# Optimization experiments

Measured on AMD Instinct MI355X. Metric: run time of the kernel, lower is better.

## Reference

```python
import jax, jax.numpy as jnp
import numpy as np

E, C_IN, NUM_CLASSES = 4, 3, 100
HW = 32
C1, C2, GC = 64, 128, 16
FC_IN = C2 * (HW // 4) * (HW // 4)  # 128*8*8 = 8192


def _conv(x, w, b):
    # x: [B,Cin,H,W], w: [Cout,Cin,3,3] -> [B,Cout,H,W] (SAME padding)
    y = jax.lax.conv_general_dilated(x, w, (1, 1), 'SAME',
                                     dimension_numbers=('NCHW', 'OIHW', 'NCHW'))
    return y + b[None, :, None, None]


def _maxpool2(x):
    return jax.lax.reduce_window(x, -jnp.inf, jax.lax.max,
                                 (1, 1, 2, 2), (1, 1, 2, 2), 'VALID')


def setup_inputs() -> dict:
    key = jax.random.key(0)
    ks = jax.random.split(key, 12)
    s = lambda k, shape, fan: (jax.random.normal(k, shape, jnp.float32) / np.sqrt(fan))
    return {
        'x': jax.random.normal(ks[0], (1024, C_IN, HW, HW), jnp.float32),
        # gating network
        'gate_cw': s(ks[1], (GC, C_IN, 3, 3), C_IN * 9),
        'gate_cb': jnp.zeros((GC,), jnp.float32),
        'gate_fw': s(ks[2], (E, GC), GC),
        'gate_fb': jnp.zeros((E,), jnp.float32),
        # stacked expert params [E, ...]
        'e_c1w': s(ks[3], (E, C1, C_IN, 3, 3), C_IN * 9),
        'e_c1b': jnp.zeros((E, C1), jnp.float32),
        'e_c2w': s(ks[4], (E, C2, C1, 3, 3), C1 * 9),
        'e_c2b': jnp.zeros((E, C2), jnp.float32),
        'e_fw': s(ks[5], (E, NUM_CLASSES, FC_IN), FC_IN),
        'e_fb': jnp.zeros((E, NUM_CLASSES), jnp.float32),
    }


def reference(x, gate_cw, gate_cb, gate_fw, gate_fb,
              e_c1w, e_c1b, e_c2w, e_c2b, e_fw, e_fb):
    B = x.shape[0]
    # --- gating: conv -> relu -> global avg pool -> linear -> softmax ---
    g = jax.nn.relu(_conv(x, gate_cw, gate_cb))            # [B,GC,H,W]
    g = g.mean(axis=(2, 3))                                # [B,GC]
    router_probs = jax.nn.softmax(g @ gate_fw.T + gate_fb) # [B,E]

    best_weights = router_probs.max(axis=1)                # [B]
    best_indices = jnp.argmax(router_probs, axis=1)        # [B]

    # --- hard top-1 dispatch: mask-and-combine (same math as gather/scatter) ---
    final_output = jnp.zeros((B, NUM_CLASSES), x.dtype)
    for e in range(E):  # fixed small expert count, structurally distinct params
        h = jax.nn.relu(_conv(x, e_c1w[e], e_c1b[e]))      # [B,64,32,32]
        h = _maxpool2(h)                                   # [B,64,16,16]
        h = jax.nn.relu(_conv(h, e_c2w[e], e_c2b[e]))      # [B,128,16,16]
        h = _maxpool2(h)                                   # [B,128,8,8]
        logits = h.reshape(B, -1) @ e_fw[e].T + e_fb[e]    # [B,100]
        mask = (best_indices == e)[:, None]
        final_output = final_output + jnp.where(
            mask, logits * best_weights[:, None], 0.0)

    mean_probs = router_probs.mean(axis=0)
    aux_loss = jnp.mean((mean_probs - 1.0 / E) ** 2)
    return final_output, router_probs, aux_loss
```

## Files before the change

kernel.cpp:

```cpp
#include <hip/hip_runtime.h>
#include <hip/hip_bf16.h>
#include <cstdint>


#define B_TOT 1024

typedef __attribute__((ext_vector_type(8))) short short8;
typedef __attribute__((ext_vector_type(16))) float f32x16;

__device__ __forceinline__ ushort f2bf(float f) {
  uint32_t u = __float_as_uint(f);
  u += 0x7fffu + ((u >> 16) & 1u);
  return (ushort)(u >> 16);
}

__global__ __launch_bounds__(256) void k_wprep(const float* __restrict__ w2,
                                               ushort* __restrict__ wp) {
  const int i = blockIdx.x * 256 + threadIdx.x;
  const int j = i & 7;
  const int cout = (i >> 3) & 127;
  const int kb = (i >> 10) & 7;
  const int kkE = i >> 13;
  const int kk = kkE - (kkE / 9) * 9;
  const int e = kkE / 9;
  const int ci = kb * 8 + j;
  const float f = w2[(size_t)(((e * 128 + cout) * 64 + ci) * 9) + kk];
  wp[i] = f2bf(f);
}

__global__ __launch_bounds__(256) void k_w1prep(const float* __restrict__ w1,
                                                ushort* __restrict__ wA) {
  const int i = blockIdx.x * 256 + threadIdx.x;
  const int j = i & 7;
  const int cout = (i >> 3) & 63;
  const int kb = (i >> 9) & 3;
  const int e = i >> 11;
  const int k = kb * 8 + j;
  float f = 0.f;
  if (k < 27) {
    const int ci = k / 9;
    const int kk = k - ci * 9;
    f = w1[(size_t)(((e * 64 + cout) * 3 + ci) * 9) + kk];
  }
  wA[i] = f2bf(f);
}

__global__ __launch_bounds__(256) void k_wfc(const float* __restrict__ efw,
                                             ushort* __restrict__ wfc) {
  const int i = blockIdx.x * 256 + threadIdx.x;
  const int j = i & 7;
  const int cout = (i >> 3) & 127;
  const int kb = (i >> 10) & 1023;
  const int e = i >> 20;
  const int k = kb * 8 + j;
  float f = 0.f;
  if (cout < 100) f = efw[((size_t)(e * 100 + cout)) * 8192 + k];
  wfc[i] = f2bf(f);
}

__global__ __launch_bounds__(256, 2) void k_gate(
    const float* __restrict__ x, const float* __restrict__ gcw,
    const float* __restrict__ gcb, float* __restrict__ g_mean) {
  __shared__ float xs[3 * 34 * 34];
  __shared__ float red[4 * 16];
  const int b = blockIdx.x;
  const int t = threadIdx.x;
  const float* xb = x + (size_t)b * 3072;

  for (int c = t; c < 3468; c += 256) {
    const int ci = c / 1156;
    const int rem = c - ci * 1156;
    const int y = rem / 34;
    const int xx = rem - y * 34;
    const int gy = y - 1, gx = xx - 1;
    float v = 0.f;
    if (gy >= 0 && gy < 32 && gx >= 0 && gx < 32) v = xb[ci * 1024 + gy * 32 + gx];
    xs[c] = v;
  }
  __syncthreads();

  const int r = t >> 3;
  const int c0 = (t & 7) * 4;

  float accp[16][4];
#pragma unroll
  for (int c = 0; c < 16; c++)
#pragma unroll
    for (int p = 0; p < 4; p++) accp[c][p] = 0.f;

#pragma unroll
  for (int ci = 0; ci < 3; ci++) {
    float pv[3][6];
#pragma unroll
    for (int dy = 0; dy < 3; dy++) {
      const float* row = xs + ci * 1156 + (r + dy) * 34 + c0;
#pragma unroll
      for (int dx = 0; dx < 6; dx++) pv[dy][dx] = row[dx];
    }
#pragma unroll
    for (int c = 0; c < 16; c++) {
      const float* wr = gcw + (c * 3 + ci) * 9;
#pragma unroll
      for (int ky = 0; ky < 3; ky++)
#pragma unroll
        for (int kx = 0; kx < 3; kx++) {
          const float wv = wr[ky * 3 + kx];
#pragma unroll
          for (int p = 0; p < 4; p++)
            accp[c][p] += wv * pv[ky][kx + p];
        }
    }
  }

  float sums[16];
#pragma unroll
  for (int c = 0; c < 16; c++) {
    const float bb = gcb[c];
    float s = 0.f;
#pragma unroll
    for (int p = 0; p < 4; p++) s += fmaxf(accp[c][p] + bb, 0.f);
    sums[c] = s;
  }

  const int wave = t >> 6, lane = t & 63;
#pragma unroll
  for (int c = 0; c < 16; c++) {
    float v = sums[c];
    for (int o = 32; o > 0; o >>= 1) v += __shfl_down(v, o);
    if (lane == 0) red[wave * 16 + c] = v;
  }
  __syncthreads();
  if (t < 16) {
    g_mean[b * 16 + t] =
        (red[t] + red[16 + t] + red[32 + t] + red[48 + t]) * (1.f / 1024.f);
  }
}

__global__ __launch_bounds__(256) void k_router(
    const float* __restrict__ g_mean, const float* __restrict__ gfw,
    const float* __restrict__ gfb, float* __restrict__ probs,
    float* __restrict__ best_w, int* __restrict__ best_idx,
    int* __restrict__ counts) {
  const int b = blockIdx.x * 256 + threadIdx.x;
  float g[16];
#pragma unroll
  for (int c = 0; c < 16; c++) g[c] = g_mean[b * 16 + c];
  float lg[4];
#pragma unroll
  for (int e = 0; e < 4; e++) {
    float s = gfb[e];
#pragma unroll
    for (int c = 0; c < 16; c++) s += g[c] * gfw[e * 16 + c];
    lg[e] = s;
  }
  float m = fmaxf(fmaxf(lg[0], lg[1]), fmaxf(lg[2], lg[3]));
  float ex[4], s = 0.f;
#pragma unroll
  for (int e = 0; e < 4; e++) { ex[e] = expf(lg[e] - m); s += ex[e]; }
  const float inv = 1.f / s;
  float p[4];
#pragma unroll
  for (int e = 0; e < 4; e++) { p[e] = ex[e] * inv; probs[b * 4 + e] = p[e]; }
  int bi = 0; float bp = p[0];
#pragma unroll
  for (int e = 1; e < 4; e++) if (p[e] > bp) { bp = p[e]; bi = e; }
  best_w[b] = bp;
  best_idx[b] = bi;
  atomicAdd(&counts[bi], 1);
}

__global__ void k_offsets(const int* __restrict__ counts, int* __restrict__ off) {
  if (threadIdx.x == 0) {
    int o = 0;
    for (int e = 0; e < 4; e++) { off[e] = o; o += ((counts[e] + 31) & ~31); }
    off[4] = o;
  }
}

__global__ __launch_bounds__(256) void k_scatter(
    const int* __restrict__ best_idx, const int* __restrict__ off,
    int* __restrict__ cnt2, int* __restrict__ order) {
  const int b = blockIdx.x * 256 + threadIdx.x;
  const int e = best_idx[b];
  const int slot = off[e] + atomicAdd(&cnt2[e], 1);
  order[slot] = b;
}

__global__ __launch_bounds__(256) void k_aux(const float* __restrict__ probs,
                                             float* __restrict__ aux_out) {
  __shared__ float red[16];
  const int t = threadIdx.x;
  const int wave = t >> 6, lane = t & 63;
  float sums[4] = {0.f, 0.f, 0.f, 0.f};
  for (int b = t; b < B_TOT; b += 256) {
#pragma unroll
    for (int e = 0; e < 4; e++) sums[e] += probs[b * 4 + e];
  }
#pragma unroll
  for (int e = 0; e < 4; e++) {
    float v = sums[e];
    for (int o = 32; o > 0; o >>= 1) v += __shfl_down(v, o);
    if (lane == 0) red[wave * 4 + e] = v;
  }
  __syncthreads();
  if (t == 0) {
    float aux = 0.f;
#pragma unroll
    for (int e = 0; e < 4; e++) {
      const float mp = (red[e] + red[4 + e] + red[8 + e] + red[12 + e]) * (1.f / 1024.f);
      const float d = mp - 0.25f;
      aux += d * d;
    }
    aux_out[0] = aux * 0.25f;
  }
}

__global__ __launch_bounds__(256) void k_conv1(
    const float* __restrict__ x, const ushort* __restrict__ wA,
    const float* __restrict__ b1, const int* __restrict__ best_idx,
    ushort* __restrict__ h1q) {
  __shared__ ushort xs[1020];
  __shared__ __align__(16) ushort Bl[256 * 32];
  const int blk = blockIdx.x;
  const int b = blk >> 2;
  const int q = blk & 3;
  const int t = threadIdx.x;
  const int e = __builtin_amdgcn_readfirstlane(best_idx[b]);
  const float* xb = x + (size_t)b * 3072;
  const float* b1e = b1 + (size_t)e * 64;

  for (int c = t; c < 1020; c += 256) {
    const int ci = c / 340;
    const int rem = c - ci * 340;
    const int hr = rem / 34;
    const int hc = rem - hr * 34;
    const int gr = 8 * q + hr - 1, gc = hc - 1;
    float v = 0.f;
    if (gr >= 0 && gr < 32 && gc >= 0 && gc < 32) v = xb[ci * 1024 + gr * 32 + gc];
    xs[c] = f2bf(v);
  }
  __syncthreads();

  {
    const int rr = t >> 5, cc = t & 31;
    ushort us[32];
#pragma unroll
    for (int k = 0; k < 32; k++) {
      ushort v = 0;
      if (k < 27) {
        const int ci = k / 9;
        const int tap = k - ci * 9;
        const int dy = tap / 3, dx = tap - dy * 3;
        v = xs[ci * 340 + (rr + dy) * 34 + cc + dx];
      }
      us[k] = v;
    }
    uint4 pk[2];
    uint* pu = (uint*)pk;
#pragma unroll
    for (int w = 0; w < 8; w++)
      pu[w] = (uint)us[w * 2] | ((uint)us[w * 2 + 1] << 16);
    *(uint4*)(Bl + t * 32) = pk[0];
    *(uint4*)(Bl + t * 32 + 8) = pk[1];
    uint4 pk2[2];
    uint* pu2 = (uint*)pk2;
#pragma unroll
    for (int w = 0; w < 8; w++)
      pu2[w] = (uint)us[16 + w * 2] | ((uint)us[16 + w * 2 + 1] << 16);
    *(uint4*)(Bl + t * 32 + 16) = pk2[0];
    *(uint4*)(Bl + t * 32 + 24) = pk2[1];
  }
  __syncthreads();

  const int lane = t & 63;
  const int wv = t >> 6;
  const int g = wv & 1;
  const int nh = wv >> 1;
  const int ln = lane & 31;
  const int half = lane >> 5;

  const short8 af0 = *(const short8*)(wA + (size_t)(((e * 4 + half) * 64) + g * 32 + ln) * 8);
  const short8 af1 = *(const short8*)(wA + (size_t)(((e * 4 + 2 + half) * 64) + g * 32 + ln) * 8);

  f32x16 acc[4];
#pragma unroll
  for (int tt = 0; tt < 4; tt++)
#pragma unroll
    for (int i = 0; i < 16; i++) acc[tt][i] = 0.f;

#pragma unroll
  for (int tt = 0; tt < 4; tt++) {
    const ushort* bcol = Bl + (size_t)((nh * 4 + tt) * 32 + ln) * 32;
    const short8 b0 = *(const short8*)(bcol + half * 8);
    const short8 b1v = *(const short8*)(bcol + 16 + half * 8);
    acc[tt] = __builtin_amdgcn_mfma_f32_32x32x16_bf16(af0, b0, acc[tt], 0, 0, 0);
    acc[tt] = __builtin_amdgcn_mfma_f32_32x32x16_bf16(af1, b1v, acc[tt], 0, 0, 0);
  }

  float bias[16];
#pragma unroll
  for (int r = 0; r < 16; r++)
    bias[r] = b1e[g * 32 + (r & 3) + 8 * (r >> 2) + 4 * half];

  const int pc = ln >> 1;
#pragma unroll
  for (int j = 0; j < 2; j++) {
    float pw[16];
#pragma unroll
    for (int r = 0; r < 16; r++) {
      float v = fmaxf(acc[2 * j][r], acc[2 * j + 1][r]);
      v = fmaxf(v, __shfl_xor(v, 1));
      pw[r] = fmaxf(v + bias[r], 0.f);
    }
    if ((lane & 1) == 0) {
      const int pos = (4 * q + nh * 2 + j) * 16 + pc;
      ushort* dst = h1q + (size_t)b * 16384 + pos * 8 + 4 * half;
#pragma unroll
      for (int rg = 0; rg < 4; rg++) {
        uint2 pk;
        pk.x = (uint)f2bf(pw[rg * 4 + 0]) | ((uint)f2bf(pw[rg * 4 + 1]) << 16);
        pk.y = (uint)f2bf(pw[rg * 4 + 2]) | ((uint)f2bf(pw[rg * 4 + 3]) << 16);
        *(uint2*)(dst + (g * 4 + rg) * 2048) = pk;
      }
    }
  }
}

__global__ __launch_bounds__(256) void k_conv2(
    const ushort* __restrict__ h1q, const ushort* __restrict__ wp,
    const float* __restrict__ b2, const int* __restrict__ best_idx,
    ushort* __restrict__ h2q) {
  __shared__ uint4 st[1440];
  const int blk = blockIdx.x;
  const int b = blk >> 1;
  const int q = blk & 1;
  const int t = threadIdx.x;
  const int e = __builtin_amdgcn_readfirstlane(best_idx[b]);
  const ushort* wpe = wp + (size_t)e * 73728;

  for (int c = t; c < 1440; c += 256) {
    const int row = c / 144;
    const int rem = c - row * 144;
    const int cig = rem / 18;
    const int col = rem - cig * 18;
    const int gy = 8 * q - 1 + row, gx = col - 1;
    uint4 v = make_uint4(0u, 0u, 0u, 0u);
    if (gy >= 0 && gy < 16 && gx >= 0 && gx < 16)
      v = *(const uint4*)(h1q + (size_t)b * 16384 + cig * 2048 + (gy * 16 + gx) * 8);
    st[c] = v;
  }
  __syncthreads();

  const int lane = t & 63;
  const int wv = t >> 6;
  const int g = wv & 1;
  const int h = wv >> 1;
  const int half = lane >> 5;
  const int n = lane & 31;
  const int drow = n >> 4;
  const int col15 = n & 15;
  const int cm0 = g * 64;

  f32x16 acc[2][2];
#pragma unroll
  for (int m = 0; m < 2; m++)
#pragma unroll
    for (int nt = 0; nt < 2; nt++)
#pragma unroll
      for (int i = 0; i < 16; i++) acc[m][nt][i] = 0.f;

  const short* sbs = (const short*)st;

  for (int kk = 0; kk < 9; kk++) {
    const int ky = kk / 3;
    const int kx = kk - ky * 3;
#pragma unroll
    for (int c4 = 0; c4 < 4; c4++) {
      const int kb = c4 * 2 + half;
      const short8 af0 = *(const short8*)(wpe + kk * 8192 +
                                          (size_t)(kb * 128 + cm0 + n) * 8);
      const short8 af1 = *(const short8*)(wpe + kk * 8192 +
                                          (size_t)(kb * 128 + cm0 + 32 + n) * 8);
#pragma unroll
      for (int nt = 0; nt < 2; nt++) {
        const int rin = 4 * h + 2 * nt + drow + ky;
        const int cin = col15 + kx;
        const short8 bf = *(const short8*)(sbs + ((rin * 8 + kb) * 18 + cin) * 8);
        acc[0][nt] = __builtin_amdgcn_mfma_f32_32x32x16_bf16(af0, bf, acc[0][nt], 0, 0, 0);
        acc[1][nt] = __builtin_amdgcn_mfma_f32_32x32x16_bf16(af1, bf, acc[1][nt], 0, 0, 0);
      }
    }
  }
  __syncthreads();

  ushort* pls = (ushort*)st;
#pragma unroll
  for (int m = 0; m < 2; m++)
#pragma unroll
    for (int nt = 0; nt < 2; nt++) {
#pragma unroll
      for (int r = 0; r < 16; r++) {
        float v = acc[m][nt][r];
        v = fmaxf(v, __shfl_xor(v, 1));
        v = fmaxf(v, __shfl_xor(v, 16));
        if ((lane & 17) == 0) {
          const int rowm = (r & 3) + 8 * (r >> 2) + 4 * half;
          const int cout = cm0 + m * 32 + rowm;
          const int prl = 2 * h + nt;
          const int pc = (n >> 1) & 7;
          pls[cout * 32 + prl * 8 + pc] = f2bf(fmaxf(v + b2[e * 128 + cout], 0.f));
        }
      }
    }
  __syncthreads();

  {
#pragma unroll
    for (int p = 0; p < 2; p++) {
      const int f16 = p * 256 + t;
      const int flat = f16 * 8;
      const int cout = flat >> 5;
      const int pos32 = flat & 31;
      uint4* dst = (uint4*)(h2q + (size_t)b * 8192 + cout * 64 + 32 * q + pos32);
      *dst = ((const uint4*)pls)[f16];
    }
  }
}

__global__ __launch_bounds__(256) void k_fc(
    const ushort* __restrict__ h2q, const ushort* __restrict__ wfc,
    const int* __restrict__ order, const int* __restrict__ off,
    const int* __restrict__ counts, float* __restrict__ partial) {
  __shared__ ushort bs[32 * 32 * 8];
  __shared__ int sid[32];
  const int tix = blockIdx.x;
  const int ks = blockIdx.y;
  const int base = tix * 32;
  if (base >= off[4]) return;
  int e = 0;
#pragma unroll
  for (int i = 1; i < 4; i++) if (base >= off[i]) e = i;
  const int vend = off[e] + counts[e];
  const int t = threadIdx.x;
  if (t < 32) {
    const int pos = base + t;
    sid[t] = (pos < vend) ? order[pos] : -1;
  }
  __syncthreads();

  const int lane = t & 63;
  const int wv = t >> 6;
  const int half = lane >> 5;
  const int mn = lane & 31;
  const int cout0 = wv * 32;
  const int ss = t & 31;
  const int kgrp = t >> 5;
  const int srow = sid[ss] >= 0 ? sid[ss] : 0;
  const ushort* arow = h2q + (size_t)srow * 8192;

  f32x16 acc;
#pragma unroll
  for (int i = 0; i < 16; i++) acc[i] = 0.f;

  const ushort* wbase = wfc + ((size_t)e * 1024 + (size_t)ks * 64) * 1024;
  const short* sb = (const short*)bs;

#pragma unroll
  for (int ch = 0; ch < 2; ch++) {
    const int k0g = ks * 512 + ch * 256;
    if (ch) __syncthreads();
#pragma unroll
    for (int p = 0; p < 4; p++) {
      const int kb = p * 8 + kgrp;
      const uint4 v = *(const uint4*)(arow + k0g + kb * 8);
      *(uint4*)(bs + (kb * 32 + ss) * 8) = v;
    }
    __syncthreads();
#pragma unroll
    for (int kk = 0; kk < 16; kk++) {
      const int kbl = kk * 2 + half;
      const short8 af = *(const short8*)(wbase +
          ((size_t)(ch * 32 + kbl) * 128 + cout0 + mn) * 8);
      const short8 bf = *(const short8*)(sb + (kbl * 32 + mn) * 8);
      acc = __builtin_amdgcn_mfma_f32_32x32x16_bf16(af, bf, acc, 0, 0, 0);
    }
  }

  float* pks = partial + (size_t)ks * 147456;
#pragma unroll
  for (int r = 0; r < 16; r++) {
    const int cout = cout0 + (r & 3) + 8 * (r >> 2) + 4 * half;
    pks[(size_t)cout * 1152 + base + mn] = acc[r];
  }
}

__global__ __launch_bounds__(256) void k_red(
    const float* __restrict__ partial, const float* __restrict__ efb,
    const int* __restrict__ order, const int* __restrict__ off,
    const int* __restrict__ counts, const float* __restrict__ best_w,
    float* __restrict__ out) {
  const int slot = blockIdx.x * 256 + threadIdx.x;
  if (slot >= off[4]) return;
  int e = 0;
#pragma unroll
  for (int i = 1; i < 4; i++) if (slot >= off[i]) e = i;
  if (slot - off[e] >= counts[e]) return;
  const int s = order[slot];
  const float bw = best_w[s];
  const int o0 = blockIdx.y * 4;
#pragma unroll
  for (int j = 0; j < 4; j++) {
    const int o = o0 + j;
    float sum = 0.f;
#pragma unroll
    for (int ks = 0; ks < 16; ks++)
      sum += partial[(size_t)ks * 147456 + (size_t)o * 1152 + slot];
    out[(size_t)s * 100 + o] = (sum + efb[e * 100 + o]) * bw;
  }
}

extern "C" void kernel_launch(void* const* d_in, const int* in_sizes, int n_in,
                              void* d_out, int out_size, void* d_ws, size_t ws_size,
                              hipStream_t stream) {
  const float* x   = (const float*)d_in[0];
  const float* gcw = (const float*)d_in[1];
  const float* gcb = (const float*)d_in[2];
  const float* gfw = (const float*)d_in[3];
  const float* gfb = (const float*)d_in[4];
  const float* c1w = (const float*)d_in[5];
  const float* c1b = (const float*)d_in[6];
  const float* c2w = (const float*)d_in[7];
  const float* c2b = (const float*)d_in[8];
  const float* efw = (const float*)d_in[9];
  const float* efb = (const float*)d_in[10];
  float* out = (float*)d_out;
  float* ws  = (float*)d_ws;

  float*  g_mean   = ws;
  float*  best_w   = ws + 16384;
  int*    best_idx = (int*)(ws + 17408);
  int*    counts   = (int*)(ws + 18432);
  int*    cnt2     = (int*)(ws + 18436);
  int*    off      = (int*)(ws + 18440);
  int*    order    = (int*)(ws + 18448);
  ushort* wp       = (ushort*)(ws + 20480);
  ushort* wfc      = (ushort*)(ws + 167936);
  ushort* h1       = (ushort*)(ws + 2265088);
  ushort* h2q      = (ushort*)(ws + 10653696);
  float*  partial  = ws + 14848000;
  ushort* wA       = (ushort*)(ws + 17207296);

  float* probs = out + 102400;
  float* aux   = out + 106496;

  hipMemsetAsync(counts, 0, 8 * sizeof(int), stream);

  k_wprep<<<1152, 256, 0, stream>>>(c2w, wp);
  k_w1prep<<<128, 256, 0, stream>>>(c1w, wA);
  k_wfc<<<16384, 256, 0, stream>>>(efw, wfc);
  k_gate<<<1024, 256, 0, stream>>>(x, gcw, gcb, g_mean);
  k_router<<<4, 256, 0, stream>>>(g_mean, gfw, gfb, probs, best_w, best_idx, counts);
  k_offsets<<<1, 64, 0, stream>>>(counts, off);
  k_scatter<<<4, 256, 0, stream>>>(best_idx, off, cnt2, order);
  k_aux<<<1, 256, 0, stream>>>(probs, aux);
  k_conv1<<<4096, 256, 0, stream>>>(x, wA, c1b, best_idx, h1);
  k_conv2<<<2048, 256, 0, stream>>>(h1, wp, c2b, best_idx, h2q);
  dim3 g5(36, 16);
  k_fc<<<g5, 256, 0, stream>>>(h2q, wfc, order, off, counts, partial);
  dim3 g6(5, 25);
  k_red<<<g6, 256, 0, stream>>>(partial, efb, order, off, counts, best_w, out);
}
```

Before: 256.1 us.

## Fuse routing kernels into one block and prefetch conv2 weight fragments

The router, offset, scatter and aux-loss kernels, plus the counter memset, are merged into a single one-block kernel that uses shared-memory counters. This removes four launches and their dependency gaps. In conv2 the A-operand weight fragments for the next kernel tap are loaded into registers before they are needed, and the 9-tap loop is fully unrolled, to hide global load latency behind the MFMAs. A launch bound requesting two blocks per CU is also added, which raises register pressure from the prefetch buffers and may limit occupancy. The fused router now runs serially on one workgroup.

```diff
diff --git a/kernel.cpp b/kernel.cpp
--- a/kernel.cpp
+++ b/kernel.cpp
@@ -136,69 +136,76 @@
   }
 }
 
-__global__ __launch_bounds__(256) void k_router(
+__global__ __launch_bounds__(256) void k_route(
     const float* __restrict__ g_mean, const float* __restrict__ gfw,
     const float* __restrict__ gfb, float* __restrict__ probs,
     float* __restrict__ best_w, int* __restrict__ best_idx,
-    int* __restrict__ counts) {
-  const int b = blockIdx.x * 256 + threadIdx.x;
-  float g[16];
-#pragma unroll
-  for (int c = 0; c < 16; c++) g[c] = g_mean[b * 16 + c];
-  float lg[4];
-#pragma unroll
-  for (int e = 0; e < 4; e++) {
-    float s = gfb[e];
-#pragma unroll
-    for (int c = 0; c < 16; c++) s += g[c] * gfw[e * 16 + c];
-    lg[e] = s;
-  }
-  float m = fmaxf(fmaxf(lg[0], lg[1]), fmaxf(lg[2], lg[3]));
-  float ex[4], s = 0.f;
-#pragma unroll
-  for (int e = 0; e < 4; e++) { ex[e] = expf(lg[e] - m); s += ex[e]; }
-  const float inv = 1.f / s;
-  float p[4];
-#pragma unroll
-  for (int e = 0; e < 4; e++) { p[e] = ex[e] * inv; probs[b * 4 + e] = p[e]; }
-  int bi = 0; float bp = p[0];
-#pragma unroll
-  for (int e = 1; e < 4; e++) if (p[e] > bp) { bp = p[e]; bi = e; }
-  best_w[b] = bp;
-  best_idx[b] = bi;
-  atomicAdd(&counts[bi], 1);
-}
-
-__global__ void k_offsets(const int* __restrict__ counts, int* __restrict__ off) {
-  if (threadIdx.x == 0) {
-    int o = 0;
-    for (int e = 0; e < 4; e++) { off[e] = o; o += ((counts[e] + 31) & ~31); }
-    off[4] = o;
-  }
-}
-
-__global__ __launch_bounds__(256) void k_scatter(
-    const int* __restrict__ best_idx, const int* __restrict__ off,
-    int* __restrict__ cnt2, int* __restrict__ order) {
-  const int b = blockIdx.x * 256 + threadIdx.x;
-  const int e = best_idx[b];
-  const int slot = off[e] + atomicAdd(&cnt2[e], 1);
-  order[slot] = b;
-}
-
-__global__ __launch_bounds__(256) void k_aux(const float* __restrict__ probs,
-                                             float* __restrict__ aux_out) {
+    int* __restrict__ off_g, int* __restrict__ counts_g,
+    int* __restrict__ order, float* __restrict__ aux_out) {
+  __shared__ int cnt[4], ofs[5], cl[4];
+  __shared__ short bidx[1024];
   __shared__ float red[16];
   const int t = threadIdx.x;
+  if (t < 4) { cnt[t] = 0; cl[t] = 0; }
+  __syncthreads();
+
+  float asum[4] = {0.f, 0.f, 0.f, 0.f};
+  for (int s = t; s < B_TOT; s += 256) {
+    float g[16];
+#pragma unroll
+    for (int c = 0; c < 16; c++) g[c] = g_mean[s * 16 + c];
+    float lg[4];
+#pragma unroll
+    for (int e = 0; e < 4; e++) {
+      float sum = gfb[e];
+#pragma unroll
+      for (int c = 0; c < 16; c++) sum += g[c] * gfw[e * 16 + c];
+      lg[e] = sum;
+    }
+    const float m = fmaxf(fmaxf(lg[0], lg[1]), fmaxf(lg[2], lg[3]));
+    float ex[4], ssum = 0.f;
+#pragma unroll
+    for (int e = 0; e < 4; e++) { ex[e] = expf(lg[e] - m); ssum += ex[e]; }
+    const float inv = 1.f / ssum;
+    float p[4];
+#pragma unroll
+    for (int e = 0; e < 4; e++) {
+      p[e] = ex[e] * inv;
+      probs[s * 4 + e] = p[e];
+      asum[e] += p[e];
+    }
+    int bi = 0; float bp = p[0];
+#pragma unroll
+    for (int e = 1; e < 4; e++) if (p[e] > bp) { bp = p[e]; bi = e; }
+    best_w[s] = bp;
+    best_idx[s] = bi;
+    bidx[s] = (short)bi;
+    atomicAdd(&cnt[bi], 1);
+  }
+  __syncthreads();
+
+  if (t == 0) {
+    int o = 0;
+#pragma unroll
+    for (int e = 0; e < 4; e++) { ofs[e] = o; o += ((cnt[e] + 31) & ~31); }
+    ofs[4] = o;
+#pragma unroll
+    for (int i = 0; i < 5; i++) off_g[i] = ofs[i];
+#pragma unroll
+    for (int e = 0; e < 4; e++) counts_g[e] = cnt[e];
+  }
+  __syncthreads();
+
+  for (int s = t; s < B_TOT; s += 256) {
+    const int e2 = bidx[s];
+    const int slot = ofs[e2] + atomicAdd(&cl[e2], 1);
+    order[slot] = s;
+  }
+
   const int wave = t >> 6, lane = t & 63;
-  float sums[4] = {0.f, 0.f, 0.f, 0.f};
-  for (int b = t; b < B_TOT; b += 256) {
-#pragma unroll
-    for (int e = 0; e < 4; e++) sums[e] += probs[b * 4 + e];
-  }
 #pragma unroll
   for (int e = 0; e < 4; e++) {
-    float v = sums[e];
+    float v = asum[e];
     for (int o = 32; o > 0; o >>= 1) v += __shfl_down(v, o);
     if (lane == 0) red[wave * 4 + e] = v;
   }
@@ -326,7 +333,7 @@
   }
 }
 
-__global__ __launch_bounds__(256) void k_conv2(
+__global__ __launch_bounds__(256, 2) void k_conv2(
     const ushort* __restrict__ h1q, const ushort* __restrict__ wp,
     const float* __restrict__ b2, const int* __restrict__ best_idx,
     ushort* __restrict__ h2q) {
@@ -370,24 +377,33 @@
       for (int i = 0; i < 16; i++) acc[m][nt][i] = 0.f;
 
   const short* sbs = (const short*)st;
-
+  const ushort* abase = wpe + (size_t)(half * 128 + cm0 + n) * 8;
+
+  short8 a0[4], a1[4];
+#pragma unroll
+  for (int c4 = 0; c4 < 4; c4++) {
+    a0[c4] = *(const short8*)(abase + c4 * 2048);
+    a1[c4] = *(const short8*)(abase + c4 * 2048 + 256);
+  }
+
+#pragma unroll
   for (int kk = 0; kk < 9; kk++) {
     const int ky = kk / 3;
     const int kx = kk - ky * 3;
 #pragma unroll
     for (int c4 = 0; c4 < 4; c4++) {
       const int kb = c4 * 2 + half;
-      const short8 af0 = *(const short8*)(wpe + kk * 8192 +
-                                          (size_t)(kb * 128 + cm0 + n) * 8);
-      const short8 af1 = *(const short8*)(wpe + kk * 8192 +
-                                          (size_t)(kb * 128 + cm0 + 32 + n) * 8);
 #pragma unroll
       for (int nt = 0; nt < 2; nt++) {
         const int rin = 4 * h + 2 * nt + drow + ky;
         const int cin = col15 + kx;
         const short8 bf = *(const short8*)(sbs + ((rin * 8 + kb) * 18 + cin) * 8);
-        acc[0][nt] = __builtin_amdgcn_mfma_f32_32x32x16_bf16(af0, bf, acc[0][nt], 0, 0, 0);
-        acc[1][nt] = __builtin_amdgcn_mfma_f32_32x32x16_bf16(af1, bf, acc[1][nt], 0, 0, 0);
+        acc[0][nt] = __builtin_amdgcn_mfma_f32_32x32x16_bf16(a0[c4], bf, acc[0][nt], 0, 0, 0);
+        acc[1][nt] = __builtin_amdgcn_mfma_f32_32x32x16_bf16(a1[c4], bf, acc[1][nt], 0, 0, 0);
+      }
+      if (kk < 8) {
+        a0[c4] = *(const short8*)(abase + (kk + 1) * 8192 + c4 * 2048);
+        a1[c4] = *(const short8*)(abase + (kk + 1) * 8192 + c4 * 2048 + 256);
       }
     }
   }
@@ -540,7 +556,6 @@
   float*  best_w   = ws + 16384;
   int*    best_idx = (int*)(ws + 17408);
   int*    counts   = (int*)(ws + 18432);
-  int*    cnt2     = (int*)(ws + 18436);
   int*    off      = (int*)(ws + 18440);
   int*    order    = (int*)(ws + 18448);
   ushort* wp       = (ushort*)(ws + 20480);
@@ -553,16 +568,12 @@
   float* probs = out + 102400;
   float* aux   = out + 106496;
 
-  hipMemsetAsync(counts, 0, 8 * sizeof(int), stream);
-
   k_wprep<<<1152, 256, 0, stream>>>(c2w, wp);
   k_w1prep<<<128, 256, 0, stream>>>(c1w, wA);
   k_wfc<<<16384, 256, 0, stream>>>(efw, wfc);
   k_gate<<<1024, 256, 0, stream>>>(x, gcw, gcb, g_mean);
-  k_router<<<4, 256, 0, stream>>>(g_mean, gfw, gfb, probs, best_w, best_idx, counts);
-  k_offsets<<<1, 64, 0, stream>>>(counts, off);
-  k_scatter<<<4, 256, 0, stream>>>(best_idx, off, cnt2, order);
-  k_aux<<<1, 256, 0, stream>>>(probs, aux);
+  k_route<<<1, 256, 0, stream>>>(g_mean, gfw, gfb, probs, best_w, best_idx,
+                                 off, counts, order, aux);
   k_conv1<<<4096, 256, 0, stream>>>(x, wA, c1b, best_idx, h1);
   k_conv2<<<2048, 256, 0, stream>>>(h1, wp, c2b, best_idx, h2q);
   dim3 g5(36, 16);
```

Measured after the change: 230.4 us. 10.0% less time.
